# Performance work log

Measured on AMD Instinct MI355X. Metric: run time of the kernel, lower is better.

Reference implementation:

```python
import jax, jax.numpy as jnp
import numpy as np
from jax import lax

B, C, H, W, D, V = 1, 32, 128, 160, 64, 5


def _make_projs():
    # proj_matrices[b, v, 0] = 4x4 extrinsics [R|t], proj_matrices[b, v, 1] = 4x4 intrinsics
    f = 800.0
    K = np.eye(4, dtype=np.float32)
    K[0, 0] = K[1, 1] = f
    K[0, 2] = W / 2.0
    K[1, 2] = H / 2.0
    projs = np.zeros((B, V, 2, 4, 4), np.float32)
    for b in range(B):
        for v in range(V):
            E = np.eye(4, dtype=np.float32)
            if v > 0:
                ang = 0.02 * v
                ca, sa = np.cos(ang), np.sin(ang)
                E[:3, :3] = np.array([[ca, 0.0, sa], [0.0, 1.0, 0.0], [-sa, 0.0, ca]], np.float32)
                E[:3, 3] = np.array([0.1 * v, 0.02 * v, 0.05 * v], np.float32)
            projs[b, v, 0] = E
            projs[b, v, 1] = K
    return jnp.asarray(projs)


def setup_inputs() -> dict:
    key = jax.random.key(0)
    ks = jax.random.split(key, 6)
    inp = {f"feat{i}": jax.random.normal(ks[i], (B, C, H, W), jnp.float32) for i in range(V)}
    inp["proj_matrices"] = _make_projs()
    inp["depth_values"] = jnp.broadcast_to(
        jnp.linspace(425.0, 935.0, D, dtype=jnp.float32)[None, :], (B, D))
    inp["num_depth"] = D
    inp["conv_w"] = jax.random.normal(ks[5], (1, C, 3, 3, 3), jnp.float32) * 0.05
    inp["conv_b"] = jnp.zeros((1,), jnp.float32)
    return inp


def _bilinear_sample(fea, px, py):
    # fea: [B,C,H,W]; px,py: [B,N] pixel coords. Bilinear, zero padding, align_corners=True.
    Bb, Cc, Hh, Ww = fea.shape
    fea_flat = fea.reshape(Bb, Cc, Hh * Ww)
    x0 = jnp.floor(px)
    y0 = jnp.floor(py)
    wx1 = px - x0
    wy1 = py - y0

    def corner(xc, yc, w):
        valid = (xc >= 0) & (xc <= Ww - 1) & (yc >= 0) & (yc <= Hh - 1)
        xi = jnp.clip(xc, 0, Ww - 1).astype(jnp.int32)
        yi = jnp.clip(yc, 0, Hh - 1).astype(jnp.int32)
        idx = yi * Ww + xi  # [B,N]
        g = jax.vmap(lambda fb, ib: fb[:, ib])(fea_flat, idx)  # [B,C,N]
        return g * (w * valid)[:, None, :]

    return (corner(x0, y0, (1 - wx1) * (1 - wy1))
            + corner(x0 + 1, y0, wx1 * (1 - wy1))
            + corner(x0, y0 + 1, (1 - wx1) * wy1)
            + corner(x0 + 1, y0 + 1, wx1 * wy1))


def _homo_warp(src_fea, src_proj, ref_proj, depth_values):
    # homo_warping_3D: warp src features into ref frustum at each depth hypothesis
    Bb, Cc, Hh, Ww = src_fea.shape
    Dd = depth_values.shape[1]
    proj = jnp.einsum('bij,bjk->bik', src_proj, jnp.linalg.inv(ref_proj))
    rot, trans = proj[:, :3, :3], proj[:, :3, 3]
    yy, xx = jnp.meshgrid(jnp.arange(Hh, dtype=src_fea.dtype),
                          jnp.arange(Ww, dtype=src_fea.dtype), indexing='ij')
    xyz = jnp.stack([xx.ravel(), yy.ravel(), jnp.ones(Hh * Ww, src_fea.dtype)])  # [3,HW]
    rot_xyz = jnp.einsum('bij,jn->bin', rot, xyz)  # [B,3,HW]
    pxyz = rot_xyz[:, :, None, :] * depth_values[:, None, :, None] + trans[:, :, None, None]  # [B,3,D,HW]
    px = (pxyz[:, 0] / pxyz[:, 2]).reshape(Bb, -1)
    py = (pxyz[:, 1] / pxyz[:, 2]).reshape(Bb, -1)
    return _bilinear_sample(src_fea, px, py).reshape(Bb, Cc, Dd, Hh, Ww)


def _fuse_proj(p):
    # p: [B,2,4,4] -> [B,4,4] with K[:3,:3] @ E[:3,:4] written into top 3 rows
    top = jnp.einsum('bij,bjk->bik', p[:, 1, :3, :3], p[:, 0, :3, :4])
    return p[:, 0].at[:, :3, :4].set(top)


def reference(feat0, feat1, feat2, feat3, feat4, proj_matrices, depth_values, num_depth, conv_w, conv_b):
    feats = [feat0, feat1, feat2, feat3, feat4]
    num_views = len(feats)
    Bb, Cc, Hh, Ww = feat0.shape
    ref_proj = _fuse_proj(proj_matrices[:, 0])
    ref_vol = jnp.broadcast_to(feat0[:, :, None, :, :], (Bb, Cc, num_depth, Hh, Ww))
    vol_sum = ref_vol
    vol_sq = ref_vol ** 2
    for v in range(1, num_views):
        src_proj = _fuse_proj(proj_matrices[:, v])
        warped = _homo_warp(feats[v], src_proj, ref_proj, depth_values)
        vol_sum = vol_sum + warped
        vol_sq = vol_sq + warped ** 2
    variance = vol_sq / num_views - (vol_sum / num_views) ** 2  # [B,C,D,H,W]
    cost = lax.conv_general_dilated(variance, conv_w, (1, 1, 1), 'SAME',
                                    dimension_numbers=('NCDHW', 'OIDHW', 'NCDHW'))
    cost = cost + conv_b[None, :, None, None, None]
    prob_volume_pre = cost[:, 0]  # squeeze channel -> [B,D,H,W]
    return jax.nn.softmax(prob_volume_pre, axis=1)
```

## Files before the change

### kernel.cpp

```cpp
#include <hip/hip_runtime.h>

#define H_ 128
#define W_ 160
#define C_ 32
#define D_ 64
#define HW_ (H_*W_)
#define DHW_ (D_*HW_)

#define TY 16
#define TX 16
#define HS 18
#define NP_ (HS*HS)

#define GSTR 28

#define FEATT_SZ (5*HW_*C_)
#define MATS_OFF FEATT_SZ
#define CW3_OFF (MATS_OFF + 64)
#define A_OFF (CW3_OFF + 1152)

using v2f = __attribute__((ext_vector_type(2))) float;

__device__ __forceinline__ v2f pk_mul(v2f a, v2f b) {
    v2f d; asm("v_pk_mul_f32 %0, %1, %2" : "=v"(d) : "v"(a), "v"(b)); return d;
}
__device__ __forceinline__ v2f pk_add(v2f a, v2f b) {
    v2f d; asm("v_pk_add_f32 %0, %1, %2" : "=v"(d) : "v"(a), "v"(b)); return d;
}
__device__ __forceinline__ v2f pk_fma(v2f a, v2f b, v2f c) {
    v2f d; asm("v_pk_fma_f32 %0, %1, %2, %3" : "=v"(d) : "v"(a), "v"(b), "v"(c)); return d;
}
__device__ __forceinline__ v2f pk_mul_blo(v2f a, v2f b) {
    v2f d; asm("v_pk_mul_f32 %0, %1, %2 op_sel:[0,0] op_sel_hi:[1,0]" : "=v"(d) : "v"(a), "v"(b)); return d;
}
__device__ __forceinline__ v2f pk_mul_bhi(v2f a, v2f b) {
    v2f d; asm("v_pk_mul_f32 %0, %1, %2 op_sel:[0,1] op_sel_hi:[1,1]" : "=v"(d) : "v"(a), "v"(b)); return d;
}
__device__ __forceinline__ v2f pk_fma_blo(v2f a, v2f b, v2f c) {
    v2f d; asm("v_pk_fma_f32 %0, %1, %2, %3 op_sel:[0,0,0] op_sel_hi:[1,0,1]" : "=v"(d) : "v"(a), "v"(b), "v"(c)); return d;
}
__device__ __forceinline__ v2f pk_fma_bhi(v2f a, v2f b, v2f c) {
    v2f d; asm("v_pk_fma_f32 %0, %1, %2, %3 op_sel:[0,1,0] op_sel_hi:[1,1,1]" : "=v"(d) : "v"(a), "v"(b), "v"(c)); return d;
}
__device__ __forceinline__ v2f pk_fma_alo(v2f a, v2f b, v2f c) {
    v2f d; asm("v_pk_fma_f32 %0, %1, %2, %3 op_sel:[0,0,0] op_sel_hi:[0,1,1]" : "=v"(d) : "v"(a), "v"(b), "v"(c)); return d;
}
__device__ __forceinline__ v2f pk_fma_ahi(v2f a, v2f b, v2f c) {
    v2f d; asm("v_pk_fma_f32 %0, %1, %2, %3 op_sel:[1,0,0] op_sel_hi:[1,1,1]" : "=v"(d) : "v"(a), "v"(b), "v"(c)); return d;
}
__device__ __forceinline__ v2f pk_fma_nsq(v2f a, v2f c) {
    v2f d; asm("v_pk_fma_f32 %0, %1, %1, %2 neg_lo:[1,0,0] neg_hi:[1,0,0]" : "=v"(d) : "v"(a), "v"(c)); return d;
}

__global__ void k_setup(const float* __restrict__ proj,
                        const float* __restrict__ convw,
                        float* __restrict__ mats,
                        float* __restrict__ cw3)
{
    const int tid = threadIdx.x;
    for (int o = tid; o < 1152; o += 64) {
        const int tap = o >> 7;
        const int r   = o & 127;
        const int c   = r >> 2;
        const int kd  = r & 3;
        cw3[o] = (kd < 3) ? convw[c*27 + kd*9 + tap] : 0.f;
    }
    if (tid != 0) return;
    double F[5][12];
    for (int v = 0; v < 5; ++v) {
        const float* E = proj + v*32;
        const float* K = proj + v*32 + 16;
        for (int i = 0; i < 3; ++i)
            for (int j = 0; j < 4; ++j) {
                double s = 0.0;
                for (int k = 0; k < 3; ++k)
                    s += (double)K[i*4+k] * (double)E[k*4+j];
                F[v][i*4+j] = s;
            }
    }
    const double m00=F[0][0], m01=F[0][1], m02=F[0][2],  t0x=F[0][3];
    const double m10=F[0][4], m11=F[0][5], m12=F[0][6],  t0y=F[0][7];
    const double m20=F[0][8], m21=F[0][9], m22=F[0][10], t0z=F[0][11];
    const double det = m00*(m11*m22-m12*m21) - m01*(m10*m22-m12*m20)
                     + m02*(m10*m21-m11*m20);
    const double id = 1.0/det;
    double inv[9];
    inv[0] = (m11*m22-m12*m21)*id; inv[1] = (m02*m21-m01*m22)*id; inv[2] = (m01*m12-m02*m11)*id;
    inv[3] = (m12*m20-m10*m22)*id; inv[4] = (m00*m22-m02*m20)*id; inv[5] = (m02*m10-m00*m12)*id;
    inv[6] = (m10*m21-m11*m20)*id; inv[7] = (m01*m20-m00*m21)*id; inv[8] = (m00*m11-m01*m10)*id;
    double it[3];
    it[0] = -(inv[0]*t0x + inv[1]*t0y + inv[2]*t0z);
    it[1] = -(inv[3]*t0x + inv[4]*t0y + inv[5]*t0z);
    it[2] = -(inv[6]*t0x + inv[7]*t0y + inv[8]*t0z);
    for (int v = 1; v < 5; ++v) {
        float* o = mats + (v-1)*12;
        for (int r = 0; r < 3; ++r) {
            for (int c = 0; c < 3; ++c) {
                double s = 0.0;
                for (int k = 0; k < 3; ++k) s += F[v][r*4+k]*inv[k*3+c];
                o[r*3+c] = (float)s;
            }
            double tr = F[v][r*4+3] + F[v][r*4+0]*it[0]
                      + F[v][r*4+1]*it[1] + F[v][r*4+2]*it[2];
            o[9+r] = (float)tr;
        }
    }
}

__global__ void k_transpose(const float* __restrict__ f0, const float* __restrict__ f1,
                            const float* __restrict__ f2, const float* __restrict__ f3,
                            const float* __restrict__ f4, float* __restrict__ ft)
{
    const int bv = blockIdx.y;
    const float* f = (bv==0) ? f0 : (bv==1) ? f1 : (bv==2) ? f2 : (bv==3) ? f3 : f4;
    float* o = ft + (size_t)bv * (HW_*C_);
    __shared__ float tile[C_][65];
    const int pix0 = blockIdx.x * 64;
    const int tid = threadIdx.x;
    const int p  = tid & 63;
    const int ci = (tid >> 6) * 8;
#pragma unroll
    for (int i = 0; i < 8; ++i)
        tile[ci + i][p] = f[(size_t)(ci + i)*HW_ + pix0 + p];
    __syncthreads();
    const int c2 = tid & 31, pg = tid >> 5;
#pragma unroll
    for (int i = 0; i < 8; ++i) {
        int p2 = pg + i*8;
        o[(size_t)(pix0 + p2)*C_ + c2] = tile[c2][p2];
    }
}

__global__ __launch_bounds__(256, 2) void k_var_conv(
    const float* __restrict__ featT, const float* __restrict__ mats,
    const float* __restrict__ depthv, const float* __restrict__ cw3,
    float* __restrict__ A)
{
    __shared__ float geo[NP_ * GSTR];
    __shared__ float vlds[NP_ * C_];
    const int tid = threadIdx.x;
    const int x0 = blockIdx.x * TX;
    const int y0 = blockIdx.y * TY;
    const int bd = blockIdx.z;
    const float depth = depthv[bd];

    {
        float cf[4][9];
#pragma unroll
        for (int v = 0; v < 4; ++v) {
            const float* mm = mats + v*12;
#pragma unroll
            for (int r = 0; r < 3; ++r) {
                cf[v][r*3+0] = mm[r*3+0]*depth;
                cf[v][r*3+1] = mm[r*3+1]*depth;
                cf[v][r*3+2] = fmaf(mm[r*3+2], depth, mm[9+r]);
            }
        }
        for (int p = tid; p < NP_; p += 256) {
            const int hy = p / HS;
            const int hx = p - hy*HS;
            const int gy = y0 - 1 + hy;
            const int gx = x0 - 1 + hx;
            const bool inimg = ((unsigned)gy < 128u) && ((unsigned)gx < 160u);
            const float vp = inimg ? 1.f : 0.f;
            const float fgx = (float)gx, fgy = (float)gy;
            const int gyc = min(max(gy, 0), H_-1);
            const int gxc = min(max(gx, 0), W_-1);
            const int refoffb = (gyc*W_ + gxc) << 7;
            float* gp = geo + p*GSTR;
#pragma unroll
            for (int v = 0; v < 4; ++v) {
                const float xx = fmaf(cf[v][0],fgx, fmaf(cf[v][1],fgy, cf[v][2]));
                const float yy = fmaf(cf[v][3],fgx, fmaf(cf[v][4],fgy, cf[v][5]));
                const float zz = fmaf(cf[v][6],fgx, fmaf(cf[v][7],fgy, cf[v][8]));
                const float rz = __builtin_amdgcn_rcpf(zz);
                const float px = xx*rz, py = yy*rz;
                const float xf = floorf(px), yf = floorf(py);
                const float wx = px - xf, wy = py - yf;
                const int xi = (int)xf, yi = (int)yf;
                const bool vx0 = (xi >=  0) & (xi <= W_-1);
                const bool vx1 = (xi >= -1) & (xi <= W_-2);
                const bool vy0 = (yi >=  0) & (yi <= H_-1);
                const bool vy1 = (yi >= -1) & (yi <= H_-2);
                const int xc0 = min(max(xi,   0), W_-1);
                const int xc1 = min(max(xi+1, 0), W_-1);
                const int yc0 = min(max(yi,   0), H_-1);
                const int yc1 = min(max(yi+1, 0), H_-1);
                const float ux = 1.f - wx, uy = 1.f - wy;
                float4 w4;
                w4.x = (inimg && vx0 && vy0) ? ux*uy : 0.f;
                w4.y = (inimg && vx1 && vy0) ? wx*uy : 0.f;
                w4.z = (inimg && vx0 && vy1) ? ux*wy : 0.f;
                w4.w = (inimg && vx1 && vy1) ? wx*wy : 0.f;
                const int offb00 = (yc0*W_ + xc0) << 7;
                const int dxb    = (xc1 - xc0) << 7;
                const int dyb    = (yc1 - yc0) << 7+6;
                const int dyb2   = (yc1 - yc0) * 20480;
                (void)dyb;
                *reinterpret_cast<float4*>(gp + v*4) = w4;
                int2 oo; oo.x = offb00; oo.y = dxb | dyb2;
                *reinterpret_cast<int2*>(gp + 16 + v*2) = oo;
            }
            float2 misc; misc.x = __int_as_float(refoffb); misc.y = vp;
            *reinterpret_cast<float2*>(gp + 24) = misc;
        }
    }
    __syncthreads();

    {
        const int q = tid & 7;
        const int lane_cb = q << 4;
        const int pg = tid >> 3;
        const char* fT = (const char*)featT;

        for (int p = pg; p < NP_; p += 32) {
            const float* gp = geo + p*GSTR;
            const float2 misc = *reinterpret_cast<const float2*>(gp + 24);
            v2f misc2 = { misc.x, misc.y };
            const int refoffb = __float_as_int(misc.x) + lane_cb;

            const float4 tr = *reinterpret_cast<const float4*>(fT + refoffb);
            v2f tlo = { tr.x, tr.y }, thi = { tr.z, tr.w };
            v2f s01 = pk_mul_bhi(tlo, misc2);
            v2f s23 = pk_mul_bhi(thi, misc2);
            v2f q01 = pk_mul(s01, tlo);
            v2f q23 = pk_mul(s23, thi);

#pragma unroll
            for (int v = 0; v < 4; ++v) {
                const float4 w4 = *reinterpret_cast<const float4*>(gp + v*4);
                const int2  oo = *reinterpret_cast<const int2*>(gp + 16 + v*2);
                const int v00 = oo.x + lane_cb;
                const int dx  = oo.y & 128;
                const int dy  = oo.y - dx;
                const char* fb = fT + (size_t)(v+1)*(HW_*C_*4);
                const float4 t00 = *reinterpret_cast<const float4*>(fb + v00);
                const float4 t10 = *reinterpret_cast<const float4*>(fb + (v00 + dx));
                const float4 t01 = *reinterpret_cast<const float4*>(fb + (v00 + dy));
                const float4 t11 = *reinterpret_cast<const float4*>(fb + (v00 + dx + dy));
                v2f w01 = { w4.x, w4.y }, w23 = { w4.z, w4.w };
                v2f a;
                a = pk_mul_blo((v2f){t00.x,t00.y}, w01);
                a = pk_fma_bhi((v2f){t10.x,t10.y}, w01, a);
                a = pk_fma_blo((v2f){t01.x,t01.y}, w23, a);
                a = pk_fma_bhi((v2f){t11.x,t11.y}, w23, a);
                s01 = pk_add(s01, a);
                q01 = pk_fma(a, a, q01);
                v2f b;
                b = pk_mul_blo((v2f){t00.z,t00.w}, w01);
                b = pk_fma_bhi((v2f){t10.z,t10.w}, w01, b);
                b = pk_fma_blo((v2f){t01.z,t01.w}, w23, b);
                b = pk_fma_bhi((v2f){t11.z,t11.w}, w23, b);
                s23 = pk_add(s23, b);
                q23 = pk_fma(b, b, q23);
            }
            const v2f c5 = { 0.2f, 0.2f };
            v2f m01 = pk_mul(s01, c5), m23 = pk_mul(s23, c5);
            v2f o01 = pk_fma_nsq(m01, pk_mul(q01, c5));
            v2f o23 = pk_fma_nsq(m23, pk_mul(q23, c5));
            float4 ov = make_float4(o01.x, o01.y, o23.x, o23.y);
            *reinterpret_cast<float4*>(vlds + p*C_ + ((q ^ (p & 7)) << 2)) = ov;
        }
    }
    __syncthreads();

    const int oy = tid >> 4;
    const int ox = tid & 15;
    v2f acc01 = { 0.f, 0.f };
    float acc2 = 0.f;
#pragma unroll
    for (int ky = 0; ky < 3; ++ky) {
#pragma unroll
        for (int kx = 0; kx < 3; ++kx) {
            const int p = (oy+ky)*HS + (ox+kx);
            const int sw = p & 7;
            const float* wt   = cw3 + (ky*3+kx)*128;
            const float* vrow = vlds + p*C_;
#pragma unroll
            for (int cq = 0; cq < 8; ++cq) {
                const float4 dv = *reinterpret_cast<const float4*>(vrow + ((cq^sw)<<2));
                const float* wc = wt + cq*16;
                v2f d01 = { dv.x, dv.y }, d23 = { dv.z, dv.w };
                const float2 wk0 = *reinterpret_cast<const float2*>(wc + 0);
                const float2 wk1 = *reinterpret_cast<const float2*>(wc + 4);
                const float2 wk2 = *reinterpret_cast<const float2*>(wc + 8);
                const float2 wk3 = *reinterpret_cast<const float2*>(wc + 12);
                acc01 = pk_fma_alo(d01, (v2f){wk0.x, wk0.y}, acc01);
                acc01 = pk_fma_ahi(d01, (v2f){wk1.x, wk1.y}, acc01);
                acc01 = pk_fma_alo(d23, (v2f){wk2.x, wk2.y}, acc01);
                acc01 = pk_fma_ahi(d23, (v2f){wk3.x, wk3.y}, acc01);
                acc2 = fmaf(dv.x, wc[2],  acc2);
                acc2 = fmaf(dv.y, wc[6],  acc2);
                acc2 = fmaf(dv.z, wc[10], acc2);
                acc2 = fmaf(dv.w, wc[14], acc2);
            }
        }
    }
    const size_t o = (size_t)bd*HW_ + (size_t)(y0+oy)*W_ + (x0+ox);
    A[o]                    = acc01.x;
    A[(size_t)DHW_ + o]     = acc01.y;
    A[2*(size_t)DHW_ + o]   = acc2;
}

__global__ void k_softmax(const float* __restrict__ A,
                          const float* __restrict__ conv_b,
                          float* __restrict__ out)
{
    const int pix = blockIdx.x*256 + threadIdx.x;
    const float bs = conv_b[0];
    float cst[D_];
#pragma unroll
    for (int d = 0; d < D_; ++d) {
        float v = A[(size_t)DHW_ + (size_t)d*HW_ + pix];
        if (d > 0)      v += A[(size_t)(d-1)*HW_ + pix];
        if (d < D_-1)   v += A[2*(size_t)DHW_ + (size_t)(d+1)*HW_ + pix];
        cst[d] = v + bs;
    }
    float m = cst[0];
#pragma unroll
    for (int d = 1; d < D_; ++d) m = fmaxf(m, cst[d]);
    float s = 0.f;
#pragma unroll
    for (int d = 0; d < D_; ++d) { cst[d] = expf(cst[d] - m); s += cst[d]; }
    const float rs = 1.0f / s;
#pragma unroll
    for (int d = 0; d < D_; ++d)
        out[(size_t)d*HW_ + pix] = cst[d]*rs;
}

extern "C" void kernel_launch(void* const* d_in, const int* in_sizes, int n_in,
                              void* d_out, int out_size, void* d_ws, size_t ws_size,
                              hipStream_t stream)
{
    const float* proj   = (const float*)d_in[5];
    const float* depth  = (const float*)d_in[6];
    const float* conv_w = (const float*)d_in[8];
    const float* conv_b = (const float*)d_in[9];

    float* ws    = (float*)d_ws;
    float* featT = ws;
    float* mats  = ws + MATS_OFF;
    float* cw3   = ws + CW3_OFF;
    float* A     = ws + A_OFF;

    k_setup<<<1, 64, 0, stream>>>(proj, conv_w, mats, cw3);
    dim3 gt(HW_/64, 5);
    k_transpose<<<gt, 256, 0, stream>>>((const float*)d_in[0], (const float*)d_in[1],
                                        (const float*)d_in[2], (const float*)d_in[3],
                                        (const float*)d_in[4], featT);
    dim3 g1(W_/TX, H_/TY, D_);
    k_var_conv<<<g1, 256, 0, stream>>>(featT, mats, depth, cw3, A);
    k_softmax<<<HW_/256, 256, 0, stream>>>(A, conv_b, (float*)d_out);
}
```

Baseline: 212.7 us.

## Chunk geometry staging to shrink LDS and raise blocks per CU

The per-pixel geometry table is now built and consumed in four chunks of 81 halo pixels instead of all 324 at once. This shrinks the geometry LDS buffer to a quarter, so launch bounds can ask for 3 resident blocks instead of 2. Geometry work is also spread one (pixel, view) pair per thread, which uses the 256 threads more evenly than one pixel per thread. In exchange there are extra barriers per chunk, and the sampling loop runs 12 partly idle iterations instead of 11. The raised launch bound also tightens the register budget.

After: 207.7 us. 2.4% less time.

```diff
diff --git a/kernel.cpp b/kernel.cpp
--- a/kernel.cpp
+++ b/kernel.cpp
@@ -11,6 +11,7 @@
 #define TX 16
 #define HS 18
 #define NP_ (HS*HS)
+#define PCHUNK 81
 
 #define GSTR 28
 
@@ -131,12 +132,12 @@
     }
 }
 
-__global__ __launch_bounds__(256, 2) void k_var_conv(
+__global__ __launch_bounds__(256, 3) void k_var_conv(
     const float* __restrict__ featT, const float* __restrict__ mats,
     const float* __restrict__ depthv, const float* __restrict__ cw3,
     float* __restrict__ A)
 {
-    __shared__ float geo[NP_ * GSTR];
+    __shared__ float geo[PCHUNK * GSTR];
     __shared__ float vlds[NP_ * C_];
     const int tid = threadIdx.x;
     const int x0 = blockIdx.x * TX;
@@ -144,76 +145,72 @@
     const int bd = blockIdx.z;
     const float depth = depthv[bd];
 
-    {
-        float cf[4][9];
-#pragma unroll
-        for (int v = 0; v < 4; ++v) {
-            const float* mm = mats + v*12;
-#pragma unroll
-            for (int r = 0; r < 3; ++r) {
-                cf[v][r*3+0] = mm[r*3+0]*depth;
-                cf[v][r*3+1] = mm[r*3+1]*depth;
-                cf[v][r*3+2] = fmaf(mm[r*3+2], depth, mm[9+r]);
-            }
-        }
-        for (int p = tid; p < NP_; p += 256) {
+    const int q = tid & 7;
+    const int lane_cb = q << 4;
+    const int pg = tid >> 3;
+    const char* fT = (const char*)featT;
+
+    for (int chunk = 0; chunk < 4; ++chunk) {
+        const int base = chunk * PCHUNK;
+
+        for (int t = tid; t < PCHUNK*4; t += 256) {
+            const int pos = t >> 2;
+            const int v   = t & 3;
+            const int p   = base + pos;
             const int hy = p / HS;
             const int hx = p - hy*HS;
             const int gy = y0 - 1 + hy;
             const int gx = x0 - 1 + hx;
             const bool inimg = ((unsigned)gy < 128u) && ((unsigned)gx < 160u);
-            const float vp = inimg ? 1.f : 0.f;
             const float fgx = (float)gx, fgy = (float)gy;
-            const int gyc = min(max(gy, 0), H_-1);
-            const int gxc = min(max(gx, 0), W_-1);
-            const int refoffb = (gyc*W_ + gxc) << 7;
-            float* gp = geo + p*GSTR;
-#pragma unroll
-            for (int v = 0; v < 4; ++v) {
-                const float xx = fmaf(cf[v][0],fgx, fmaf(cf[v][1],fgy, cf[v][2]));
-                const float yy = fmaf(cf[v][3],fgx, fmaf(cf[v][4],fgy, cf[v][5]));
-                const float zz = fmaf(cf[v][6],fgx, fmaf(cf[v][7],fgy, cf[v][8]));
-                const float rz = __builtin_amdgcn_rcpf(zz);
-                const float px = xx*rz, py = yy*rz;
-                const float xf = floorf(px), yf = floorf(py);
-                const float wx = px - xf, wy = py - yf;
-                const int xi = (int)xf, yi = (int)yf;
-                const bool vx0 = (xi >=  0) & (xi <= W_-1);
-                const bool vx1 = (xi >= -1) & (xi <= W_-2);
-                const bool vy0 = (yi >=  0) & (yi <= H_-1);
-                const bool vy1 = (yi >= -1) & (yi <= H_-2);
-                const int xc0 = min(max(xi,   0), W_-1);
-                const int xc1 = min(max(xi+1, 0), W_-1);
-                const int yc0 = min(max(yi,   0), H_-1);
-                const int yc1 = min(max(yi+1, 0), H_-1);
-                const float ux = 1.f - wx, uy = 1.f - wy;
-                float4 w4;
-                w4.x = (inimg && vx0 && vy0) ? ux*uy : 0.f;
-                w4.y = (inimg && vx1 && vy0) ? wx*uy : 0.f;
-                w4.z = (inimg && vx0 && vy1) ? ux*wy : 0.f;
-                w4.w = (inimg && vx1 && vy1) ? wx*wy : 0.f;
-                const int offb00 = (yc0*W_ + xc0) << 7;
-                const int dxb    = (xc1 - xc0) << 7;
-                const int dyb    = (yc1 - yc0) << 7+6;
-                const int dyb2   = (yc1 - yc0) * 20480;
-                (void)dyb;
-                *reinterpret_cast<float4*>(gp + v*4) = w4;
-                int2 oo; oo.x = offb00; oo.y = dxb | dyb2;
-                *reinterpret_cast<int2*>(gp + 16 + v*2) = oo;
-            }
-            float2 misc; misc.x = __int_as_float(refoffb); misc.y = vp;
-            *reinterpret_cast<float2*>(gp + 24) = misc;
+            float* gp = geo + pos*GSTR;
+
+            const float* mm = mats + v*12;
+            const float c0 = mm[0]*depth, c1 = mm[1]*depth, c2 = fmaf(mm[2], depth, mm[9]);
+            const float c3 = mm[3]*depth, c4 = mm[4]*depth, c5 = fmaf(mm[5], depth, mm[10]);
+            const float c6 = mm[6]*depth, c7 = mm[7]*depth, c8 = fmaf(mm[8], depth, mm[11]);
+
+            const float xx = fmaf(c0,fgx, fmaf(c1,fgy, c2));
+            const float yy = fmaf(c3,fgx, fmaf(c4,fgy, c5));
+            const float zz = fmaf(c6,fgx, fmaf(c7,fgy, c8));
+            const float rz = __builtin_amdgcn_rcpf(zz);
+            const float px = xx*rz, py = yy*rz;
+            const float xf = floorf(px), yf = floorf(py);
+            const float wx = px - xf, wy = py - yf;
+            const int xi = (int)xf, yi = (int)yf;
+            const bool vx0 = (xi >=  0) & (xi <= W_-1);
+            const bool vx1 = (xi >= -1) & (xi <= W_-2);
+            const bool vy0 = (yi >=  0) & (yi <= H_-1);
+            const bool vy1 = (yi >= -1) & (yi <= H_-2);
+            const int xc0 = min(max(xi,   0), W_-1);
+            const int xc1 = min(max(xi+1, 0), W_-1);
+            const int yc0 = min(max(yi,   0), H_-1);
+            const int yc1 = min(max(yi+1, 0), H_-1);
+            const float ux = 1.f - wx, uy = 1.f - wy;
+            float4 w4;
+            w4.x = (inimg && vx0 && vy0) ? ux*uy : 0.f;
+            w4.y = (inimg && vx1 && vy0) ? wx*uy : 0.f;
+            w4.z = (inimg && vx0 && vy1) ? ux*wy : 0.f;
+            w4.w = (inimg && vx1 && vy1) ? wx*wy : 0.f;
+            const int offb00 = (yc0*W_ + xc0) << 7;
+            const int dxb    = (xc1 - xc0) << 7;
+            const int dyb    = (yc1 - yc0) * 20480;
+            *reinterpret_cast<float4*>(gp + v*4) = w4;
+            int2 oo; oo.x = offb00; oo.y = dxb | dyb;
+            *reinterpret_cast<int2*>(gp + 16 + v*2) = oo;
+            if (v == 0) {
+                const int gyc = min(max(gy, 0), H_-1);
+                const int gxc = min(max(gx, 0), W_-1);
+                float2 misc;
+                misc.x = __int_as_float((gyc*W_ + gxc) << 7);
+                misc.y = inimg ? 1.f : 0.f;
+                *reinterpret_cast<float2*>(gp + 24) = misc;
+            }
         }
-    }
-    __syncthreads();
-
-    {
-        const int q = tid & 7;
-        const int lane_cb = q << 4;
-        const int pg = tid >> 3;
-        const char* fT = (const char*)featT;
-
-        for (int p = pg; p < NP_; p += 32) {
+        __syncthreads();
+
+        for (int p = pg; p < PCHUNK; p += 32) {
+            const int ap = base + p;
             const float* gp = geo + p*GSTR;
             const float2 misc = *reinterpret_cast<const float2*>(gp + 24);
             v2f misc2 = { misc.x, misc.y };
@@ -259,10 +256,10 @@
             v2f o01 = pk_fma_nsq(m01, pk_mul(q01, c5));
             v2f o23 = pk_fma_nsq(m23, pk_mul(q23, c5));
             float4 ov = make_float4(o01.x, o01.y, o23.x, o23.y);
-            *reinterpret_cast<float4*>(vlds + p*C_ + ((q ^ (p & 7)) << 2)) = ov;
+            *reinterpret_cast<float4*>(vlds + ap*C_ + ((q ^ (ap & 7)) << 2)) = ov;
         }
-    }
-    __syncthreads();
+        __syncthreads();
+    }
 
     const int oy = tid >> 4;
     const int ox = tid & 15;
```

## Fuse geometry into sampling loop, drop geo LDS, raise occupancy, remap grid

Applied to the files above, without the earlier changes.

The separate geometry pass that wrote per-pixel bilinear weights and offsets to shared memory is removed. Each of the 8 lanes per halo pixel now recomputes the projection and weights inline before gathering. This frees about 36 KB of LDS and one barrier, and launch bounds rise from 2 to 3 blocks per CU. The grid becomes 1D with y-tiles varying fastest to improve L2 locality across neighbouring blocks. The cost is that the projection math is done 8 times per pixel, and register pressure may rise under the tighter bound.

Measured after the change: 209.5 us. Within noise of the previous version (-1.5%).

```diff
diff --git a/kernel.cpp b/kernel.cpp
--- a/kernel.cpp
+++ b/kernel.cpp
@@ -11,8 +11,6 @@
 #define TX 16
 #define HS 18
 #define NP_ (HS*HS)
-
-#define GSTR 28
 
 #define FEATT_SZ (5*HW_*C_)
 #define MATS_OFF FEATT_SZ
@@ -131,136 +129,112 @@
     }
 }
 
-__global__ __launch_bounds__(256, 2) void k_var_conv(
+__global__ __launch_bounds__(256, 3) void k_var_conv(
     const float* __restrict__ featT, const float* __restrict__ mats,
     const float* __restrict__ depthv, const float* __restrict__ cw3,
     float* __restrict__ A)
 {
-    __shared__ float geo[NP_ * GSTR];
     __shared__ float vlds[NP_ * C_];
     const int tid = threadIdx.x;
-    const int x0 = blockIdx.x * TX;
-    const int y0 = blockIdx.y * TY;
-    const int bd = blockIdx.z;
+    const int n  = blockIdx.x;
+    const int y0 = (n & 7) * TY;
+    const int t  = n >> 3;
+    const int x0 = (t % 10) * TX;
+    const int bd = t / 10;
     const float depth = depthv[bd];
 
-    {
-        float cf[4][9];
+    const int q = tid & 7;
+    const int lane_cb = q << 4;
+    const int pg = tid >> 3;
+    const char* fT = (const char*)featT;
+
+    float cf[4][9];
+#pragma unroll
+    for (int v = 0; v < 4; ++v) {
+        const float* mm = mats + v*12;
+#pragma unroll
+        for (int r = 0; r < 3; ++r) {
+            cf[v][r*3+0] = mm[r*3+0]*depth;
+            cf[v][r*3+1] = mm[r*3+1]*depth;
+            cf[v][r*3+2] = fmaf(mm[r*3+2], depth, mm[9+r]);
+        }
+    }
+
+    for (int p = pg; p < NP_; p += 32) {
+        const int hy = p / HS;
+        const int hx = p - hy*HS;
+        const int gy = y0 - 1 + hy;
+        const int gx = x0 - 1 + hx;
+        const bool inimg = ((unsigned)gy < 128u) && ((unsigned)gx < 160u);
+        const float vp = inimg ? 1.f : 0.f;
+        const float fgx = (float)gx, fgy = (float)gy;
+
+        const int gyc = min(max(gy, 0), H_-1);
+        const int gxc = min(max(gx, 0), W_-1);
+        const float4 tr = *reinterpret_cast<const float4*>(fT + (((gyc*W_ + gxc) << 7) + lane_cb));
+        const v2f vp2 = { vp, vp };
+        v2f tlo = { tr.x, tr.y }, thi = { tr.z, tr.w };
+        v2f s01 = pk_mul(tlo, vp2);
+        v2f s23 = pk_mul(thi, vp2);
+        v2f q01 = pk_mul(s01, tlo);
+        v2f q23 = pk_mul(s23, thi);
+
 #pragma unroll
         for (int v = 0; v < 4; ++v) {
-            const float* mm = mats + v*12;
-#pragma unroll
-            for (int r = 0; r < 3; ++r) {
-                cf[v][r*3+0] = mm[r*3+0]*depth;
-                cf[v][r*3+1] = mm[r*3+1]*depth;
-                cf[v][r*3+2] = fmaf(mm[r*3+2], depth, mm[9+r]);
-            }
+            const float xx = fmaf(cf[v][0],fgx, fmaf(cf[v][1],fgy, cf[v][2]));
+            const float yy = fmaf(cf[v][3],fgx, fmaf(cf[v][4],fgy, cf[v][5]));
+            const float zz = fmaf(cf[v][6],fgx, fmaf(cf[v][7],fgy, cf[v][8]));
+            const float rz = __builtin_amdgcn_rcpf(zz);
+            const float px = xx*rz, py = yy*rz;
+            const float xf = floorf(px), yf = floorf(py);
+            const float wx = px - xf, wy = py - yf;
+            const int xi = (int)xf, yi = (int)yf;
+            const bool vx0 = (xi >=  0) & (xi <= W_-1);
+            const bool vx1 = (xi >= -1) & (xi <= W_-2);
+            const bool vy0 = (yi >=  0) & (yi <= H_-1);
+            const bool vy1 = (yi >= -1) & (yi <= H_-2);
+            const int xc0 = min(max(xi,   0), W_-1);
+            const int xc1 = min(max(xi+1, 0), W_-1);
+            const int yc0 = min(max(yi,   0), H_-1);
+            const int yc1 = min(max(yi+1, 0), H_-1);
+            const float ux = 1.f - wx, uy = 1.f - wy;
+            float4 w4;
+            w4.x = (inimg && vx0 && vy0) ? ux*uy : 0.f;
+            w4.y = (inimg && vx1 && vy0) ? wx*uy : 0.f;
+            w4.z = (inimg && vx0 && vy1) ? ux*wy : 0.f;
+            w4.w = (inimg && vx1 && vy1) ? wx*wy : 0.f;
+            const int off00 = ((yc0*W_ + xc0) << 7) + lane_cb;
+            const int dxb   = (xc1 - xc0) << 7;
+            const int dyb   = (yc1 - yc0) * 20480;
+
+            const char* fb = fT + (size_t)(v+1)*(HW_*C_*4);
+            const float4 t00 = *reinterpret_cast<const float4*>(fb + off00);
+            const float4 t10 = *reinterpret_cast<const float4*>(fb + (off00 + dxb));
+            const float4 t01 = *reinterpret_cast<const float4*>(fb + (off00 + dyb));
+            const float4 t11 = *reinterpret_cast<const float4*>(fb + (off00 + dxb + dyb));
+
+            v2f w01 = { w4.x, w4.y }, w23 = { w4.z, w4.w };
+            v2f a;
+            a = pk_mul_blo((v2f){t00.x,t00.y}, w01);
+            a = pk_fma_bhi((v2f){t10.x,t10.y}, w01, a);
+            a = pk_fma_blo((v2f){t01.x,t01.y}, w23, a);
+            a = pk_fma_bhi((v2f){t11.x,t11.y}, w23, a);
+            s01 = pk_add(s01, a);
+            q01 = pk_fma(a, a, q01);
+            v2f b;
+            b = pk_mul_blo((v2f){t00.z,t00.w}, w01);
+            b = pk_fma_bhi((v2f){t10.z,t10.w}, w01, b);
+            b = pk_fma_blo((v2f){t01.z,t01.w}, w23, b);
+            b = pk_fma_bhi((v2f){t11.z,t11.w}, w23, b);
+            s23 = pk_add(s23, b);
+            q23 = pk_fma(b, b, q23);
         }
-        for (int p = tid; p < NP_; p += 256) {
-            const int hy = p / HS;
-            const int hx = p - hy*HS;
-            const int gy = y0 - 1 + hy;
-            const int gx = x0 - 1 + hx;
-            const bool inimg = ((unsigned)gy < 128u) && ((unsigned)gx < 160u);
-            const float vp = inimg ? 1.f : 0.f;
-            const float fgx = (float)gx, fgy = (float)gy;
-            const int gyc = min(max(gy, 0), H_-1);
-            const int gxc = min(max(gx, 0), W_-1);
-            const int refoffb = (gyc*W_ + gxc) << 7;
-            float* gp = geo + p*GSTR;
-#pragma unroll
-            for (int v = 0; v < 4; ++v) {
-                const float xx = fmaf(cf[v][0],fgx, fmaf(cf[v][1],fgy, cf[v][2]));
-                const float yy = fmaf(cf[v][3],fgx, fmaf(cf[v][4],fgy, cf[v][5]));
-                const float zz = fmaf(cf[v][6],fgx, fmaf(cf[v][7],fgy, cf[v][8]));
-                const float rz = __builtin_amdgcn_rcpf(zz);
-                const float px = xx*rz, py = yy*rz;
-                const float xf = floorf(px), yf = floorf(py);
-                const float wx = px - xf, wy = py - yf;
-                const int xi = (int)xf, yi = (int)yf;
-                const bool vx0 = (xi >=  0) & (xi <= W_-1);
-                const bool vx1 = (xi >= -1) & (xi <= W_-2);
-                const bool vy0 = (yi >=  0) & (yi <= H_-1);
-                const bool vy1 = (yi >= -1) & (yi <= H_-2);
-                const int xc0 = min(max(xi,   0), W_-1);
-                const int xc1 = min(max(xi+1, 0), W_-1);
-                const int yc0 = min(max(yi,   0), H_-1);
-                const int yc1 = min(max(yi+1, 0), H_-1);
-                const float ux = 1.f - wx, uy = 1.f - wy;
-                float4 w4;
-                w4.x = (inimg && vx0 && vy0) ? ux*uy : 0.f;
-                w4.y = (inimg && vx1 && vy0) ? wx*uy : 0.f;
-                w4.z = (inimg && vx0 && vy1) ? ux*wy : 0.f;
-                w4.w = (inimg && vx1 && vy1) ? wx*wy : 0.f;
-                const int offb00 = (yc0*W_ + xc0) << 7;
-                const int dxb    = (xc1 - xc0) << 7;
-                const int dyb    = (yc1 - yc0) << 7+6;
-                const int dyb2   = (yc1 - yc0) * 20480;
-                (void)dyb;
-                *reinterpret_cast<float4*>(gp + v*4) = w4;
-                int2 oo; oo.x = offb00; oo.y = dxb | dyb2;
-                *reinterpret_cast<int2*>(gp + 16 + v*2) = oo;
-            }
-            float2 misc; misc.x = __int_as_float(refoffb); misc.y = vp;
-            *reinterpret_cast<float2*>(gp + 24) = misc;
-        }
-    }
-    __syncthreads();
-
-    {
-        const int q = tid & 7;
-        const int lane_cb = q << 4;
-        const int pg = tid >> 3;
-        const char* fT = (const char*)featT;
-
-        for (int p = pg; p < NP_; p += 32) {
-            const float* gp = geo + p*GSTR;
-            const float2 misc = *reinterpret_cast<const float2*>(gp + 24);
-            v2f misc2 = { misc.x, misc.y };
-            const int refoffb = __float_as_int(misc.x) + lane_cb;
-
-            const float4 tr = *reinterpret_cast<const float4*>(fT + refoffb);
-            v2f tlo = { tr.x, tr.y }, thi = { tr.z, tr.w };
-            v2f s01 = pk_mul_bhi(tlo, misc2);
-            v2f s23 = pk_mul_bhi(thi, misc2);
-            v2f q01 = pk_mul(s01, tlo);
-            v2f q23 = pk_mul(s23, thi);
-
-#pragma unroll
-            for (int v = 0; v < 4; ++v) {
-                const float4 w4 = *reinterpret_cast<const float4*>(gp + v*4);
-                const int2  oo = *reinterpret_cast<const int2*>(gp + 16 + v*2);
-                const int v00 = oo.x + lane_cb;
-                const int dx  = oo.y & 128;
-                const int dy  = oo.y - dx;
-                const char* fb = fT + (size_t)(v+1)*(HW_*C_*4);
-                const float4 t00 = *reinterpret_cast<const float4*>(fb + v00);
-                const float4 t10 = *reinterpret_cast<const float4*>(fb + (v00 + dx));
-                const float4 t01 = *reinterpret_cast<const float4*>(fb + (v00 + dy));
-                const float4 t11 = *reinterpret_cast<const float4*>(fb + (v00 + dx + dy));
-                v2f w01 = { w4.x, w4.y }, w23 = { w4.z, w4.w };
-                v2f a;
-                a = pk_mul_blo((v2f){t00.x,t00.y}, w01);
-                a = pk_fma_bhi((v2f){t10.x,t10.y}, w01, a);
-                a = pk_fma_blo((v2f){t01.x,t01.y}, w23, a);
-                a = pk_fma_bhi((v2f){t11.x,t11.y}, w23, a);
-                s01 = pk_add(s01, a);
-                q01 = pk_fma(a, a, q01);
-                v2f b;
-                b = pk_mul_blo((v2f){t00.z,t00.w}, w01);
-                b = pk_fma_bhi((v2f){t10.z,t10.w}, w01, b);
-                b = pk_fma_blo((v2f){t01.z,t01.w}, w23, b);
-                b = pk_fma_bhi((v2f){t11.z,t11.w}, w23, b);
-                s23 = pk_add(s23, b);
-                q23 = pk_fma(b, b, q23);
-            }
-            const v2f c5 = { 0.2f, 0.2f };
-            v2f m01 = pk_mul(s01, c5), m23 = pk_mul(s23, c5);
-            v2f o01 = pk_fma_nsq(m01, pk_mul(q01, c5));
-            v2f o23 = pk_fma_nsq(m23, pk_mul(q23, c5));
-            float4 ov = make_float4(o01.x, o01.y, o23.x, o23.y);
-            *reinterpret_cast<float4*>(vlds + p*C_ + ((q ^ (p & 7)) << 2)) = ov;
-        }
+        const v2f c5 = { 0.2f, 0.2f };
+        v2f m01 = pk_mul(s01, c5), m23 = pk_mul(s23, c5);
+        v2f o01 = pk_fma_nsq(m01, pk_mul(q01, c5));
+        v2f o23 = pk_fma_nsq(m23, pk_mul(q23, c5));
+        float4 ov = make_float4(o01.x, o01.y, o23.x, o23.y);
+        *reinterpret_cast<float4*>(vlds + p*C_ + ((q ^ (p & 7)) << 2)) = ov;
     }
     __syncthreads();
 
@@ -348,7 +322,6 @@
     k_transpose<<<gt, 256, 0, stream>>>((const float*)d_in[0], (const float*)d_in[1],
                                         (const float*)d_in[2], (const float*)d_in[3],
                                         (const float*)d_in[4], featT);
-    dim3 g1(W_/TX, H_/TY, D_);
-    k_var_conv<<<g1, 256, 0, stream>>>(featT, mats, depth, cw3, A);
+    k_var_conv<<<(W_/TX)*(H_/TY)*D_, 256, 0, stream>>>(featT, mats, depth, cw3, A);
     k_softmax<<<HW_/256, 256, 0, stream>>>(A, conv_b, (float*)d_out);
 }
```
